# Performance work log

Hardware: AMD Instinct MI355X
Metric: run time of the kernel (lower is better)

Reference implementation:

```python
import jax, jax.numpy as jnp
import numpy as np

B = 256; M = 6; H = 448; INC = 448; EMB = 32; NHEAD = 8; DFF = 2048
OBS = 20; HOR = 30
D = EMB + 4 * NHEAD + INC      # transformer d_model = 512 (requires INC == hidden_dim)
LBUF = OBS + HOR               # 50-token buffer; index 49 is written but never read
HD = D // NHEAD
FUS_IN = D + 7 + INC           # fusion layer input = 71 + 2*hidden_dim


def _ln(x, g, b):
    mu = x.mean(-1, keepdims=True)
    var = ((x - mu) ** 2).mean(-1, keepdims=True)
    return (x - mu) * jax.lax.rsqrt(var + 1e-5) * g + b


def setup_inputs() -> dict:
    key = jax.random.key(0)
    ks = jax.random.split(key, 16)
    s = jnp.float32(0.02)
    n = lambda i, shp: jax.random.normal(ks[i], shp, dtype=jnp.float32)
    return {
        "feat_in": n(0, (B, 1, INC)),
        "loc_in": n(1, (B, M, 2)),
        "obs_trajs": n(2, (OBS, B, 2)),
        "W_emb": n(3, (2, EMB)) * s, "b_emb": jnp.zeros((EMB,)),
        "W_qkv": n(4, (D, 3 * D)) * s, "b_qkv": jnp.zeros((3 * D,)),
        "W_o": n(5, (D, D)) * s, "b_o": jnp.zeros((D,)),
        "W_ff1": n(6, (D, DFF)) * s, "b_ff1": jnp.zeros((DFF,)),
        "W_ff2": n(7, (DFF, D)) * s, "b_ff2": jnp.zeros((D,)),
        "ln1_g": jnp.ones((D,)), "ln1_b": jnp.zeros((D,)),
        "ln2_g": jnp.ones((D,)), "ln2_b": jnp.zeros((D,)),
        "W_fus": n(8, (FUS_IN, H)) * s, "b_fus": jnp.zeros((H,)),
        "W_out": n(9, (H, 2)) * s, "b_out": jnp.zeros((2,)),
    }


def reference(feat_in, loc_in, obs_trajs, W_emb, b_emb, W_qkv, b_qkv, W_o, b_o,
              W_ff1, b_ff1, W_ff2, b_ff2, ln1_g, ln1_b, ln2_g, ln2_b,
              W_fus, b_fus, W_out, b_out):
    feat = feat_in[:, 0]                                     # [B, INC]
    emb_obs = jax.nn.relu(obs_trajs @ W_emb + b_emb)         # [OBS, B, EMB]
    pos0 = jnp.zeros((LBUF, B, 2), feat.dtype).at[:OBS].set(obs_trajs)
    emb0 = jnp.zeros((LBUF, B, EMB), feat.dtype).at[:OBS].set(emb_obs)
    idxs = jnp.arange(OBS, OBS + HOR)
    scale = 1.0 / jnp.sqrt(jnp.float32(HD))
    rep = NHEAD // 2

    def run_sample(goal):                                    # goal: [B, 2]
        def step(carry, frame_idx):
            pos, emb = carry
            last = pos[frame_idx - 1]                        # [B, 2]
            dist = goal - last
            tcol = jnp.zeros((B, 1), feat.dtype) + frame_idx
            # order matches torch.cat: (emb, goal, last, dist, time, feat)
            extras = jnp.concatenate([jnp.tile(goal, (1, rep)), jnp.tile(last, (1, rep)),
                                      jnp.tile(dist, (1, rep)), jnp.tile(tcol, (1, NHEAD))], -1)
            x = jnp.concatenate([emb,
                                 jnp.broadcast_to(extras, (LBUF, B, 4 * NHEAD)),
                                 jnp.broadcast_to(feat, (LBUF, B, INC))], -1)   # [LBUF, B, D]
            qkv = x @ W_qkv + b_qkv
            q, k, v = jnp.split(qkv, 3, axis=-1)
            qh = q[frame_idx - 1].reshape(B, NHEAD, HD)      # only last query needed
            kh = k.reshape(LBUF, B, NHEAD, HD)
            vh = v.reshape(LBUF, B, NHEAD, HD)
            scores = jnp.einsum('bhd,lbhd->bhl', qh, kh) * scale
            valid = jnp.arange(LBUF) < frame_idx             # tokens 0..frame_idx-1 exist
            scores = jnp.where(valid[None, None, :], scores, -1e9)
            attn = jax.nn.softmax(scores, axis=-1)
            ctx = jnp.einsum('bhl,lbhd->bhd', attn, vh).reshape(B, D)
            a = ctx @ W_o + b_o
            x_last = x[frame_idx - 1]
            h1 = _ln(x_last + a, ln1_g, ln1_b)               # post-LN encoder layer (eval, no dropout)
            ff = jax.nn.relu(h1 @ W_ff1 + b_ff1) @ W_ff2 + b_ff2
            h2 = _ln(h1 + ff, ln2_g, ln2_b)
            fus = jnp.concatenate([h2, last, goal, dist, tcol, feat], -1)       # [B, FUS_IN]
            out = (fus @ W_fus + b_fus) @ W_out + b_out                         # [B, 2]
            pos = pos.at[frame_idx].set(out)
            emb = emb.at[frame_idx].set(jax.nn.relu(out @ W_emb + b_emb))
            return (pos, emb), out
        _, ys = jax.lax.scan(step, (pos0, emb0), idxs)
        return ys                                            # [HOR, B, 2]

    ys = jax.vmap(run_sample, in_axes=1)(loc_in)             # [M, HOR, B, 2]
    return ys.transpose(2, 0, 1, 3).reshape(B, M, HOR * 2)
```

## Files before the change

### kernel.cpp

```cpp
#include <hip/hip_runtime.h>
#include <math.h>

#define B_   256
#define N_   1536
#define OBS_ 20
#define HOR_ 30

typedef __bf16 bf16;
typedef bf16  bf16x8 __attribute__((ext_vector_type(8)));
typedef float f32x4  __attribute__((ext_vector_type(4)));

__device__ __forceinline__ void dev_gemm(
    const float* __restrict__ A, int lda,
    const float* __restrict__ Bw, int ldb,
    float* __restrict__ C, bf16* __restrict__ Cb, int ldc,
    int K, const float* __restrict__ colBias,
    int by, int bx, float* smem)
{
    float (*As)[36] = (float(*)[36])smem;
    float (*Bs)[68] = (float(*)[68])(smem + 16 * 36);
    const int tid = threadIdx.x;
    const int n0 = by * 32, j0 = bx * 64;
    const int a_k = tid & 15, a_r = tid >> 4;
    const int b_j = tid & 63, b_k = tid >> 6;
    const int tx = tid & 15, ty = tid >> 4;
    float acc[2][4] = {};
    float pa0 = A[(size_t)(n0 + a_r) * lda + a_k];
    float pa1 = A[(size_t)(n0 + a_r + 16) * lda + a_k];
    float pb[4];
#pragma unroll
    for (int i = 0; i < 4; i++) pb[i] = Bw[(size_t)(b_k + 4 * i) * ldb + j0 + b_j];
    for (int k0 = 0; k0 < K; k0 += 16) {
        As[a_k][a_r] = pa0;
        As[a_k][a_r + 16] = pa1;
#pragma unroll
        for (int i = 0; i < 4; i++) Bs[b_k + 4 * i][b_j] = pb[i];
        __syncthreads();
        if (k0 + 16 < K) {
            pa0 = A[(size_t)(n0 + a_r) * lda + k0 + 16 + a_k];
            pa1 = A[(size_t)(n0 + a_r + 16) * lda + k0 + 16 + a_k];
#pragma unroll
            for (int i = 0; i < 4; i++)
                pb[i] = Bw[(size_t)(k0 + 16 + b_k + 4 * i) * ldb + j0 + b_j];
        }
#pragma unroll
        for (int kk = 0; kk < 16; kk++) {
            float a0 = As[kk][ty * 2];
            float a1 = As[kk][ty * 2 + 1];
            float4 bv = *(const float4*)&Bs[kk][tx * 4];
            float bb[4] = {bv.x, bv.y, bv.z, bv.w};
#pragma unroll
            for (int j = 0; j < 4; j++) { acc[0][j] += a0 * bb[j]; acc[1][j] += a1 * bb[j]; }
        }
        __syncthreads();
    }
#pragma unroll
    for (int i = 0; i < 2; i++) {
        int n = n0 + ty * 2 + i;
#pragma unroll
        for (int j = 0; j < 4; j++) {
            int jj = j0 + tx * 4 + j;
            float v = acc[i][j];
            if (colBias) v += colBias[jj];
            if (C)  C[(size_t)n * ldc + jj] = v;
            if (Cb) Cb[(size_t)n * ldc + jj] = (bf16)v;
        }
    }
}

__device__ __forceinline__ void dev_pack(
    int bi, const float* __restrict__ srcF, const bf16* __restrict__ srcB,
    int srcRows, int KC, int J, int lds, bf16* __restrict__ dst)
{
    int idx = bi * 256 + threadIdx.x;
    int total = (J / 16) * KC * 64;
    if (idx >= total) return;
    int lane = idx & 63;
    int kc = (idx >> 6) % KC;
    int jg = idx / (64 * KC);
    int k0 = kc * 32 + (lane >> 4) * 8;
    int col = jg * 16 + (lane & 15);
    bf16x8 v;
#pragma unroll
    for (int i = 0; i < 8; i++) {
        int r = k0 + i;
        float x = 0.f;
        if (r < srcRows) x = srcF ? srcF[(size_t)r * lds + col] : (float)srcB[(size_t)r * lds + col];
        v[i] = (bf16)x;
    }
    *(bf16x8*)&dst[(size_t)idx * 8] = v;
}

__device__ __forceinline__ void dev_emb_obs(
    int bi, const float* __restrict__ obs, const float* __restrict__ Wemb,
    const float* __restrict__ bemb, float* __restrict__ emb_obs)
{
    int tid = bi * 256 + threadIdx.x;
    if (tid >= OBS_ * B_ * 32) return;
    int r = tid >> 5, e = tid & 31;
    float v = obs[r * 2] * Wemb[e] + obs[r * 2 + 1] * Wemb[32 + e] + bemb[e];
    emb_obs[tid] = fmaxf(v, 0.f);
}

__device__ __forceinline__ void dev_weff(
    int r, const float* __restrict__ Wqkv, const float* __restrict__ bqkv,
    float* __restrict__ Weff, float* smem)
{
    float* qrow = smem;
    const int t = threadIdx.x;
    for (int j = t; j < 512; j += 256)
        qrow[j] = (r < 512) ? Wqkv[(size_t)r * 1536 + j] : bqkv[j];
    __syncthreads();
    const int h = t >> 5, c = t & 31;
    float acc = 0.f;
#pragma unroll 8
    for (int d = 0; d < 64; d++)
        acc += qrow[h * 64 + d] * Wqkv[(size_t)c * 1536 + 512 + h * 64 + d];
    Weff[(size_t)r * 256 + t] = acc;
}

__device__ __forceinline__ void dev_wov(
    int row, const float* __restrict__ Wqkv, const float* __restrict__ Wo,
    bf16* __restrict__ WovCat, float* smem)
{
    float* vrow = smem;
    const int h = row >> 5, c = row & 31;
    const int t = threadIdx.x;
    if (t < 64) vrow[t] = Wqkv[(size_t)c * 1536 + 1024 + h * 64 + t];
    __syncthreads();
    for (int j = t; j < 512; j += 256) {
        float acc = 0.f;
#pragma unroll 8
        for (int d = 0; d < 64; d++)
            acc += vrow[d] * Wo[(size_t)(h * 64 + d) * 512 + j];
        WovCat[(size_t)row * 512 + j] = (bf16)acc;
    }
}

__global__ __launch_bounds__(256) void prologue1_k(
    const float* __restrict__ obs, const float* __restrict__ Wemb,
    const float* __restrict__ bemb, float* __restrict__ emb_obs,
    const float* __restrict__ Wqkv, const float* __restrict__ bqkv,
    float* __restrict__ Weff,
    const float* __restrict__ Wo, bf16* __restrict__ WovCat,
    const float* __restrict__ feat, float* __restrict__ featv,
    const float* __restrict__ Wfus, const float* __restrict__ bfus,
    float* __restrict__ feat_fus,
    const float* __restrict__ Wff1, bf16* __restrict__ BpF1,
    const float* __restrict__ Wff2, bf16* __restrict__ BpF2,
    bf16* __restrict__ BpFus)
{
    __shared__ __attribute__((aligned(16))) float smem[16 * 36 + 16 * 68];
    const int b = blockIdx.x;
    if (b < 640) {
        dev_emb_obs(b, obs, Wemb, bemb, emb_obs);
    } else if (b < 1153) {
        dev_weff(b - 640, Wqkv, bqkv, Weff, smem);
    } else if (b < 1409) {
        dev_wov(b - 1153, Wqkv, Wo, WovCat, smem);
    } else if (b < 1473) {
        int i = b - 1409;
        dev_gemm(feat, 448, Wqkv + 64 * 1536 + 1024, 1536,
                 featv, nullptr, 512, 448, bqkv + 1024, i >> 3, i & 7, smem);
    } else if (b < 1489) {
        int i = b - 1473;
        dev_gemm(Wqkv + 32 * 1536 + 1024, 1536, Wo, 512,
                 nullptr, WovCat + 256 * 512, 512, 512, nullptr, i >> 3, i & 7, smem);
    } else if (b < 1545) {
        int i = b - 1489;
        dev_gemm(feat, 448, Wfus + 519 * 448, 448,
                 feat_fus, nullptr, 448, 448, bfus, i / 7, i % 7, smem);
    } else if (b < 2057) {
        dev_pack(b - 1545, Wff1, nullptr, 512, 16, 2048, 2048, BpF1);
    } else if (b < 2569) {
        dev_pack(b - 2057, Wff2, nullptr, 2048, 64, 512, 512, BpF2);
    } else {
        dev_pack(b - 2569, Wfus, nullptr, 519, 17, 448, 448, BpFus);
    }
}

__global__ __launch_bounds__(256) void prologue2_k(
    const float* __restrict__ feat, const float* __restrict__ Weff,
    float* __restrict__ featqp,
    const float* __restrict__ featv, const float* __restrict__ Wo,
    const float* __restrict__ b_o, float* __restrict__ featvO,
    const bf16* __restrict__ WovCat, bf16* __restrict__ BpA)
{
    __shared__ __attribute__((aligned(16))) float smem[16 * 36 + 16 * 68];
    const int b = blockIdx.x;
    if (b < 32) {
        int i = b;
        dev_gemm(feat, 448, Weff + 64 * 256, 256,
                 featqp, nullptr, 256, 448, Weff + 512 * 256, i >> 2, i & 3, smem);
    } else if (b < 96) {
        int i = b - 32;
        dev_gemm(featv, 512, Wo, 512,
                 featvO, nullptr, 512, 512, b_o, i >> 3, i & 7, smem);
    } else {
        dev_pack(b - 96, nullptr, WovCat, 288, 9, 512, 512, BpA);
    }
}

template<int KC>
__global__ __launch_bounds__(256) void fgemm_k(
    const bf16* __restrict__ A, int lda,
    const bf16* __restrict__ Bp,
    float* __restrict__ C, bf16* __restrict__ Cb, int ldc,
    const float* __restrict__ colBias,
    const float* __restrict__ rowMat, int ldRm,
    int doRelu)
{
    const int n0 = blockIdx.y * 32;
    const int j0g = blockIdx.x * 4;
    const int tid = threadIdx.x;
    const int w = tid >> 6, lane = tid & 63;
    const int quad = lane >> 4, m15 = lane & 15;
    const int r0 = (w & 1) * 16;
    const int cg = (w >> 1) * 2;
    const bf16* Arow = &A[(size_t)(n0 + r0 + m15) * lda + quad * 8];
    const bf16* B0 = &Bp[((size_t)(j0g + cg) * KC * 64 + lane) * 8];
    const bf16* B1 = &Bp[((size_t)(j0g + cg + 1) * KC * 64 + lane) * 8];
    f32x4 acc0 = {}, acc1 = {};
#pragma unroll 8
    for (int kc = 0; kc < KC; kc++) {
        bf16x8 af = *(const bf16x8*)&Arow[kc * 32];
        bf16x8 b0 = *(const bf16x8*)&B0[(size_t)kc * 512];
        bf16x8 b1 = *(const bf16x8*)&B1[(size_t)kc * 512];
        acc0 = __builtin_amdgcn_mfma_f32_16x16x32_bf16(af, b0, acc0, 0, 0, 0);
        acc1 = __builtin_amdgcn_mfma_f32_16x16x32_bf16(af, b1, acc1, 0, 0, 0);
    }
#pragma unroll
    for (int g = 0; g < 2; g++) {
        f32x4 a = g ? acc1 : acc0;
        int j = (j0g + cg + g) * 16 + m15;
        float cb = colBias ? colBias[j] : 0.f;
#pragma unroll
        for (int r = 0; r < 4; r++) {
            int n = n0 + r0 + quad * 4 + r;
            float v = a[r] + cb;
            if (rowMat) v += rowMat[(size_t)(n / 6) * ldRm + j];
            if (doRelu) v = fmaxf(v, 0.f);
            if (C)  C[(size_t)n * ldc + j] = v;
            if (Cb) Cb[(size_t)n * ldc + j] = (bf16)v;
        }
    }
}

__global__ __launch_bounds__(256) void attn_k(
    const float* __restrict__ qp, const float* __restrict__ emb_obs,
    const float* __restrict__ emb_gen, bf16* __restrict__ ecA1b, int t)
{
    __shared__ float qp_s[256];
    __shared__ float emb_s[50 * 33];
    __shared__ float at_s[4][64];
    const int n = blockIdx.x, b = n / 6, tid = threadIdx.x;
    qp_s[tid] = qp[(size_t)n * 256 + tid];
    for (int idx = tid; idx < t * 32; idx += 256) {
        int l = idx >> 5, c = idx & 31;
        emb_s[l * 33 + c] = (l < OBS_) ? emb_obs[((size_t)l * B_ + b) * 32 + c]
                                       : emb_gen[((size_t)(l - OBS_) * N_ + n) * 32 + c];
    }
    __syncthreads();
    const int w = tid >> 6, lane = tid & 63;
#pragma unroll
    for (int hh = 0; hh < 2; hh++) {
        const int h = w * 2 + hh;
        float sc = -1e30f;
        if (lane < t) {
            float s_ = 0.f;
#pragma unroll 8
            for (int c = 0; c < 32; c++) s_ += emb_s[lane * 33 + c] * qp_s[h * 32 + c];
            sc = s_ * 0.125f;
        }
        float mx = sc;
#pragma unroll
        for (int o = 32; o > 0; o >>= 1) mx = fmaxf(mx, __shfl_xor(mx, o, 64));
        float e = (lane < t) ? __expf(sc - mx) : 0.f;
        float sm = e;
#pragma unroll
        for (int o = 32; o > 0; o >>= 1) sm += __shfl_xor(sm, o, 64);
        at_s[w][lane] = e / sm;
        if (lane < 32) {
            float ec = 0.f;
            for (int l = 0; l < t; l++) ec += at_s[w][l] * emb_s[l * 33 + lane];
            ecA1b[(size_t)n * 288 + h * 32 + lane] = (bf16)ec;
        }
    }
}

__global__ __launch_bounds__(256) void ln1_k(
    const float* __restrict__ a, const float* __restrict__ A1f,
    const float* __restrict__ feat, const float* __restrict__ g,
    const float* __restrict__ bt, float* __restrict__ h1f, bf16* __restrict__ h1b)
{
    __shared__ float red[8];
    const int n = blockIdx.x, b = n / 6, tid = threadIdx.x;
    float r[2]; float s = 0.f, sq = 0.f;
#pragma unroll
    for (int i = 0; i < 2; i++) {
        int j = tid + i * 256;
        float x = (j < 64) ? A1f[(size_t)n * 64 + j] : feat[(size_t)b * 448 + (j - 64)];
        float v = a[(size_t)n * 512 + j] + x;
        r[i] = v; s += v; sq += v * v;
    }
#pragma unroll
    for (int o = 32; o > 0; o >>= 1) { s += __shfl_xor(s, o, 64); sq += __shfl_xor(sq, o, 64); }
    int w = tid >> 6, lane = tid & 63;
    if (lane == 0) { red[w] = s; red[4 + w] = sq; }
    __syncthreads();
    s  = red[0] + red[1] + red[2] + red[3];
    sq = red[4] + red[5] + red[6] + red[7];
    float mu = s * (1.f / 512.f);
    float var = sq * (1.f / 512.f) - mu * mu;
    float rs = rsqrtf(var + 1e-5f);
#pragma unroll
    for (int i = 0; i < 2; i++) {
        int j = tid + i * 256;
        float v = (r[i] - mu) * rs * g[j] + bt[j];
        h1f[(size_t)n * 512 + j] = v;
        h1b[(size_t)n * 512 + j] = (bf16)v;
    }
}

__global__ __launch_bounds__(256) void ln2_k(
    const float* __restrict__ h1, const float* __restrict__ ff,
    const float* __restrict__ g, const float* __restrict__ bt,
    const float* __restrict__ small5, bf16* __restrict__ h2p)
{
    __shared__ float red[8];
    const int n = blockIdx.x, tid = threadIdx.x;
    float r[2]; float s = 0.f, sq = 0.f;
#pragma unroll
    for (int i = 0; i < 2; i++) {
        int j = tid + i * 256;
        float v = h1[(size_t)n * 512 + j] + ff[(size_t)n * 512 + j];
        r[i] = v; s += v; sq += v * v;
    }
#pragma unroll
    for (int o = 32; o > 0; o >>= 1) { s += __shfl_xor(s, o, 64); sq += __shfl_xor(sq, o, 64); }
    int w = tid >> 6, lane = tid & 63;
    if (lane == 0) { red[w] = s; red[4 + w] = sq; }
    __syncthreads();
    s  = red[0] + red[1] + red[2] + red[3];
    sq = red[4] + red[5] + red[6] + red[7];
    float mu = s * (1.f / 512.f);
    float var = sq * (1.f / 512.f) - mu * mu;
    float rs = rsqrtf(var + 1e-5f);
#pragma unroll
    for (int i = 0; i < 2; i++) {
        int j = tid + i * 256;
        h2p[(size_t)n * 544 + j] = (bf16)((r[i] - mu) * rs * g[j] + bt[j]);
    }
    if (tid < 7)  h2p[(size_t)n * 544 + 512 + tid] = (bf16)small5[n * 8 + tid];
    if (tid < 25) h2p[(size_t)n * 544 + 519 + tid] = (bf16)0.f;
}

__device__ __forceinline__ void next_state(
    int n, int b, int t, float o0, float o1, float g0, float g1, float tc,
    const float* Wemb, const float* bemb, const float* Weff, const float* featqp,
    float* emb_dst, float* A1f, bf16* ecA1b, float* small5, float* qp, float* A1s)
{
    float d0 = g0 - o0, d1 = g1 - o1;
    if (t < 32) {
        float e = fmaxf(o0 * Wemb[t] + o1 * Wemb[32 + t] + bemb[t], 0.f);
        if (emb_dst) emb_dst[t] = e;
        A1s[t] = e;
    } else if (t < 64) {
        int c = t - 32;
        float v;
        if      (c < 8)  v = (c & 1) ? g1 : g0;
        else if (c < 16) v = (c & 1) ? o1 : o0;
        else if (c < 24) v = (c & 1) ? d1 : d0;
        else             v = tc;
        A1s[t] = v;
    }
    if (t < 7) {
        float v2 = (t==0)?o0:(t==1)?o1:(t==2)?g0:(t==3)?g1:(t==4)?d0:(t==5)?d1:tc;
        small5[n * 8 + t] = v2;
    }
    __syncthreads();
    if (t < 64) {
        A1f[(size_t)n * 64 + t] = A1s[t];
        if (t >= 32) ecA1b[(size_t)n * 288 + 256 + (t - 32)] = (bf16)A1s[t];
    }
    float acc = featqp[(size_t)b * 256 + t];
#pragma unroll 8
    for (int k = 0; k < 64; k++) acc += A1s[k] * Weff[k * 256 + t];
    qp[(size_t)n * 256 + t] = acc;
}

__global__ __launch_bounds__(256) void init_k(
    const float* __restrict__ obs, const float* __restrict__ emb_obs,
    const float* __restrict__ loc, const float* __restrict__ Weff,
    const float* __restrict__ featqp,
    float* __restrict__ A1f, bf16* __restrict__ ecA1b,
    float* __restrict__ small5, float* __restrict__ qp)
{
    __shared__ float A1s[64];
    const int n = blockIdx.x, b = n / 6, m = n % 6, t = threadIdx.x;
    float o0 = obs[(19 * B_ + b) * 2], o1 = obs[(19 * B_ + b) * 2 + 1];
    float g0 = loc[b * 12 + m * 2], g1 = loc[b * 12 + m * 2 + 1];
    if (t < 32) {
        A1s[t] = emb_obs[((size_t)19 * B_ + b) * 32 + t];
    } else if (t < 64) {
        int c = t - 32; float d0 = g0 - o0, d1 = g1 - o1; float tc = 20.f;
        float v;
        if      (c < 8)  v = (c & 1) ? g1 : g0;
        else if (c < 16) v = (c & 1) ? o1 : o0;
        else if (c < 24) v = (c & 1) ? d1 : d0;
        else             v = tc;
        A1s[t] = v;
    }
    if (t < 7) {
        float d0 = g0 - o0, d1 = g1 - o1; float tc = 20.f;
        float v2 = (t==0)?o0:(t==1)?o1:(t==2)?g0:(t==3)?g1:(t==4)?d0:(t==5)?d1:tc;
        small5[n * 8 + t] = v2;
    }
    __syncthreads();
    if (t < 64) {
        A1f[(size_t)n * 64 + t] = A1s[t];
        if (t >= 32) ecA1b[(size_t)n * 288 + 256 + (t - 32)] = (bf16)A1s[t];
    }
    float acc = featqp[(size_t)b * 256 + t];
#pragma unroll 8
    for (int k = 0; k < 64; k++) acc += A1s[k] * Weff[k * 256 + t];
    qp[(size_t)n * 256 + t] = acc;
}

__global__ __launch_bounds__(256) void finish_k(
    const float* __restrict__ fusv, const float* __restrict__ Wout,
    const float* __restrict__ bout, const float* __restrict__ Wemb,
    const float* __restrict__ bemb, const float* __restrict__ loc,
    const float* __restrict__ Weff, const float* __restrict__ featqp,
    float* __restrict__ dout, float* __restrict__ emb_gen,
    float* __restrict__ A1f, bf16* __restrict__ ecA1b,
    float* __restrict__ small5, float* __restrict__ qp, int s)
{
    __shared__ float red[8];
    __shared__ float osh[2];
    __shared__ float A1s[64];
    const int n = blockIdx.x, b = n / 6, m = n % 6, t = threadIdx.x;
    float f0 = fusv[(size_t)n * 448 + t];
    float p0 = f0 * Wout[t * 2];
    float p1 = f0 * Wout[t * 2 + 1];
    if (t < 192) {
        float f1 = fusv[(size_t)n * 448 + 256 + t];
        p0 += f1 * Wout[(256 + t) * 2];
        p1 += f1 * Wout[(256 + t) * 2 + 1];
    }
#pragma unroll
    for (int o = 32; o > 0; o >>= 1) { p0 += __shfl_xor(p0, o, 64); p1 += __shfl_xor(p1, o, 64); }
    int w = t >> 6, lane = t & 63;
    if (lane == 0) { red[w] = p0; red[4 + w] = p1; }
    __syncthreads();
    if (t == 0) {
        float o0 = red[0] + red[1] + red[2] + red[3] + bout[0];
        float o1 = red[4] + red[5] + red[6] + red[7] + bout[1];
        osh[0] = o0; osh[1] = o1;
        dout[(size_t)b * 360 + m * 60 + s * 2]     = o0;
        dout[(size_t)b * 360 + m * 60 + s * 2 + 1] = o1;
    }
    __syncthreads();
    float o0 = osh[0], o1 = osh[1];
    float g0 = loc[b * 12 + m * 2], g1 = loc[b * 12 + m * 2 + 1];
    next_state(n, b, t, o0, o1, g0, g1, (float)(OBS_ + s + 1),
               Wemb, bemb, Weff, featqp,
               &emb_gen[((size_t)s * N_ + n) * 32], A1f, ecA1b, small5, qp, A1s);
}

extern "C" void kernel_launch(void* const* d_in, const int* in_sizes, int n_in,
                              void* d_out_, int out_size, void* d_ws, size_t ws_size,
                              hipStream_t stream) {
    (void)in_sizes; (void)n_in; (void)out_size; (void)ws_size;
    const float* feat  = (const float*)d_in[0];
    const float* loc   = (const float*)d_in[1];
    const float* obs   = (const float*)d_in[2];
    const float* W_emb = (const float*)d_in[3];
    const float* b_emb = (const float*)d_in[4];
    const float* W_qkv = (const float*)d_in[5];
    const float* b_qkv = (const float*)d_in[6];
    const float* W_o   = (const float*)d_in[7];
    const float* b_o   = (const float*)d_in[8];
    const float* W_ff1 = (const float*)d_in[9];
    const float* b_ff1 = (const float*)d_in[10];
    const float* W_ff2 = (const float*)d_in[11];
    const float* b_ff2 = (const float*)d_in[12];
    const float* ln1_g = (const float*)d_in[13];
    const float* ln1_b = (const float*)d_in[14];
    const float* ln2_g = (const float*)d_in[15];
    const float* ln2_b = (const float*)d_in[16];
    const float* W_fus = (const float*)d_in[17];
    const float* b_fus = (const float*)d_in[18];
    const float* W_out = (const float*)d_in[19];
    const float* b_out = (const float*)d_in[20];
    float* dout = (float*)d_out_;

    float* ws = (float*)d_ws;
    float* Weff     = ws; ws += 513 * 256;
    float* featqp   = ws; ws += 256 * 256;
    float* featv    = ws; ws += 256 * 512;
    float* featvO   = ws; ws += 256 * 512;
    float* feat_fus = ws; ws += 256 * 448;
    float* emb_obs  = ws; ws += OBS_ * B_ * 32;
    float* emb_gen  = ws; ws += HOR_ * N_ * 32;
    float* qp       = ws; ws += (size_t)N_ * 256;
    float* A1f      = ws; ws += (size_t)N_ * 64;
    float* small5   = ws; ws += (size_t)N_ * 8;
    float* h1f      = ws; ws += (size_t)N_ * 512;
    float* aF       = ws; ws += (size_t)N_ * 512;
    float* ffB      = ws; ws += (size_t)N_ * 512;
    float* fusv     = ws; ws += (size_t)N_ * 448;
    bf16* WovCat = (bf16*)ws; ws += (320 * 512) / 2;
    bf16* BpA    = (bf16*)ws; ws += (32 * 9 * 512) / 2;
    bf16* BpF1   = (bf16*)ws; ws += (128 * 16 * 512) / 2;
    bf16* BpF2   = (bf16*)ws; ws += (32 * 64 * 512) / 2;
    bf16* BpFus  = (bf16*)ws; ws += (28 * 17 * 512) / 2;
    bf16* ecA1b  = (bf16*)ws; ws += ((size_t)N_ * 288) / 2;
    bf16* h1b    = (bf16*)ws; ws += ((size_t)N_ * 512) / 2;
    bf16* f1b    = (bf16*)ws; ws += ((size_t)N_ * 2048) / 2;
    bf16* h2p    = (bf16*)ws; ws += ((size_t)N_ * 544) / 2;

    prologue1_k<<<dim3(2688), dim3(256), 0, stream>>>(
        obs, W_emb, b_emb, emb_obs, W_qkv, b_qkv, Weff, W_o, WovCat,
        feat, featv, W_fus, b_fus, feat_fus, W_ff1, BpF1, W_ff2, BpF2, BpFus);
    prologue2_k<<<dim3(168), dim3(256), 0, stream>>>(
        feat, Weff, featqp, featv, W_o, b_o, featvO, WovCat, BpA);
    init_k<<<dim3(N_), dim3(256), 0, stream>>>(obs, emb_obs, loc, Weff, featqp,
        A1f, ecA1b, small5, qp);

    for (int s = 0; s < HOR_; s++) {
        attn_k<<<dim3(N_), dim3(256), 0, stream>>>(qp, emb_obs, emb_gen, ecA1b, OBS_ + s);
        fgemm_k<9><<<dim3(8, 48), dim3(256), 0, stream>>>(ecA1b, 288, BpA,
            aF, nullptr, 512, nullptr, featvO, 512, 0);
        ln1_k<<<dim3(N_), dim3(256), 0, stream>>>(aF, A1f, feat, ln1_g, ln1_b, h1f, h1b);
        fgemm_k<16><<<dim3(32, 48), dim3(256), 0, stream>>>(h1b, 512, BpF1,
            nullptr, f1b, 2048, b_ff1, nullptr, 0, 1);
        fgemm_k<64><<<dim3(8, 48), dim3(256), 0, stream>>>(f1b, 2048, BpF2,
            ffB, nullptr, 512, b_ff2, nullptr, 0, 0);
        ln2_k<<<dim3(N_), dim3(256), 0, stream>>>(h1f, ffB, ln2_g, ln2_b, small5, h2p);
        fgemm_k<17><<<dim3(7, 48), dim3(256), 0, stream>>>(h2p, 544, BpFus,
            fusv, nullptr, 448, nullptr, feat_fus, 448, 0);
        finish_k<<<dim3(N_), dim3(256), 0, stream>>>(fusv, W_out, b_out, W_emb, b_emb,
            loc, Weff, featqp, dout, emb_gen, A1f, ecA1b, small5, qp, s);
    }
}
```

Before: 2.686 ms.

## Fuse step-finish into attention and LayerNorm2 into fusion GEMM

Folds the per-step output projection, embedding update and query recompute (formerly finish_k) into the start of the next step's attention kernel, with one trailing finish_k after the loop. Also fuses LayerNorm2 into the fusion-layer MFMA GEMM, so the normalized bf16 rows stay in shared memory instead of going through a global h2p buffer. This removes two kernel launches per step and one global round-trip of activations. In exchange, LN2 is recomputed redundantly across the 7 column blocks, and the attention kernel carries extra serial work.

```diff
diff --git a/kernel.cpp b/kernel.cpp
--- a/kernel.cpp
+++ b/kernel.cpp
@@ -246,27 +246,100 @@
     }
 }
 
-__global__ __launch_bounds__(256) void attn_k(
-    const float* __restrict__ qp, const float* __restrict__ emb_obs,
-    const float* __restrict__ emb_gen, bf16* __restrict__ ecA1b, int t)
+__global__ __launch_bounds__(256) void attn2_k(
+    const float* __restrict__ qp_g,
+    const float* __restrict__ emb_obs,
+    float* __restrict__ emb_gen,
+    const float* __restrict__ fusv,
+    const float* __restrict__ Wout, const float* __restrict__ bout,
+    const float* __restrict__ Wemb, const float* __restrict__ bemb,
+    const float* __restrict__ loc,
+    const float* __restrict__ Weff, const float* __restrict__ featqp,
+    float* __restrict__ dout,
+    float* __restrict__ A1f, bf16* __restrict__ ecA1b,
+    float* __restrict__ small5, int s)
 {
     __shared__ float qp_s[256];
     __shared__ float emb_s[50 * 33];
     __shared__ float at_s[4][64];
-    const int n = blockIdx.x, b = n / 6, tid = threadIdx.x;
-    qp_s[tid] = qp[(size_t)n * 256 + tid];
-    for (int idx = tid; idx < t * 32; idx += 256) {
+    __shared__ float red[8];
+    __shared__ float osh[2];
+    __shared__ float A1s[64];
+    const int n = blockIdx.x, b = n / 6, m = n % 6, tid = threadIdx.x;
+    const int tlen = OBS_ + s;
+
+    if (s == 0) {
+        qp_s[tid] = qp_g[(size_t)n * 256 + tid];
+    } else {
+        float f0 = fusv[(size_t)n * 448 + tid];
+        float p0 = f0 * Wout[tid * 2];
+        float p1 = f0 * Wout[tid * 2 + 1];
+        if (tid < 192) {
+            float f1 = fusv[(size_t)n * 448 + 256 + tid];
+            p0 += f1 * Wout[(256 + tid) * 2];
+            p1 += f1 * Wout[(256 + tid) * 2 + 1];
+        }
+#pragma unroll
+        for (int o = 32; o > 0; o >>= 1) { p0 += __shfl_xor(p0, o, 64); p1 += __shfl_xor(p1, o, 64); }
+        int w = tid >> 6, lane = tid & 63;
+        if (lane == 0) { red[w] = p0; red[4 + w] = p1; }
+        __syncthreads();
+        if (tid == 0) {
+            float o0 = red[0] + red[1] + red[2] + red[3] + bout[0];
+            float o1 = red[4] + red[5] + red[6] + red[7] + bout[1];
+            osh[0] = o0; osh[1] = o1;
+            dout[(size_t)b * 360 + m * 60 + (s - 1) * 2]     = o0;
+            dout[(size_t)b * 360 + m * 60 + (s - 1) * 2 + 1] = o1;
+        }
+        __syncthreads();
+        float o0 = osh[0], o1 = osh[1];
+        float g0 = loc[b * 12 + m * 2], g1 = loc[b * 12 + m * 2 + 1];
+        float d0 = g0 - o0, d1 = g1 - o1;
+        float tc = (float)(OBS_ + s);
+        if (tid < 32) {
+            float e = fmaxf(o0 * Wemb[tid] + o1 * Wemb[32 + tid] + bemb[tid], 0.f);
+            emb_gen[((size_t)(s - 1) * N_ + n) * 32 + tid] = e;
+            A1s[tid] = e;
+        } else if (tid < 64) {
+            int c = tid - 32;
+            float v;
+            if      (c < 8)  v = (c & 1) ? g1 : g0;
+            else if (c < 16) v = (c & 1) ? o1 : o0;
+            else if (c < 24) v = (c & 1) ? d1 : d0;
+            else             v = tc;
+            A1s[tid] = v;
+        }
+        if (tid < 7) {
+            float v2 = (tid==0)?o0:(tid==1)?o1:(tid==2)?g0:(tid==3)?g1:(tid==4)?d0:(tid==5)?d1:tc;
+            small5[n * 8 + tid] = v2;
+        }
+        __syncthreads();
+        if (tid < 64) {
+            A1f[(size_t)n * 64 + tid] = A1s[tid];
+            if (tid >= 32) ecA1b[(size_t)n * 288 + 256 + (tid - 32)] = (bf16)A1s[tid];
+        }
+        float acc = featqp[(size_t)b * 256 + tid];
+#pragma unroll 8
+        for (int k = 0; k < 64; k++) acc += A1s[k] * Weff[k * 256 + tid];
+        qp_s[tid] = acc;
+    }
+
+    for (int idx = tid; idx < tlen * 32; idx += 256) {
         int l = idx >> 5, c = idx & 31;
-        emb_s[l * 33 + c] = (l < OBS_) ? emb_obs[((size_t)l * B_ + b) * 32 + c]
-                                       : emb_gen[((size_t)(l - OBS_) * N_ + n) * 32 + c];
-    }
-    __syncthreads();
+        float v;
+        if (l < OBS_)                 v = emb_obs[((size_t)l * B_ + b) * 32 + c];
+        else if (l == tlen - 1)       v = A1s[c];
+        else                          v = emb_gen[((size_t)(l - OBS_) * N_ + n) * 32 + c];
+        emb_s[l * 33 + c] = v;
+    }
+    __syncthreads();
+
     const int w = tid >> 6, lane = tid & 63;
 #pragma unroll
     for (int hh = 0; hh < 2; hh++) {
         const int h = w * 2 + hh;
         float sc = -1e30f;
-        if (lane < t) {
+        if (lane < tlen) {
             float s_ = 0.f;
 #pragma unroll 8
             for (int c = 0; c < 32; c++) s_ += emb_s[lane * 33 + c] * qp_s[h * 32 + c];
@@ -275,14 +348,14 @@
         float mx = sc;
 #pragma unroll
         for (int o = 32; o > 0; o >>= 1) mx = fmaxf(mx, __shfl_xor(mx, o, 64));
-        float e = (lane < t) ? __expf(sc - mx) : 0.f;
+        float e = (lane < tlen) ? __expf(sc - mx) : 0.f;
         float sm = e;
 #pragma unroll
         for (int o = 32; o > 0; o >>= 1) sm += __shfl_xor(sm, o, 64);
         at_s[w][lane] = e / sm;
         if (lane < 32) {
             float ec = 0.f;
-            for (int l = 0; l < t; l++) ec += at_s[w][l] * emb_s[l * 33 + lane];
+            for (int l = 0; l < tlen; l++) ec += at_s[w][l] * emb_s[l * 33 + lane];
             ecA1b[(size_t)n * 288 + h * 32 + lane] = (bf16)ec;
         }
     }
@@ -322,37 +395,76 @@
     }
 }
 
-__global__ __launch_bounds__(256) void ln2_k(
-    const float* __restrict__ h1, const float* __restrict__ ff,
-    const float* __restrict__ g, const float* __restrict__ bt,
-    const float* __restrict__ small5, bf16* __restrict__ h2p)
-{
-    __shared__ float red[8];
-    const int n = blockIdx.x, tid = threadIdx.x;
-    float r[2]; float s = 0.f, sq = 0.f;
-#pragma unroll
-    for (int i = 0; i < 2; i++) {
-        int j = tid + i * 256;
-        float v = h1[(size_t)n * 512 + j] + ff[(size_t)n * 512 + j];
-        r[i] = v; s += v; sq += v * v;
-    }
-#pragma unroll
-    for (int o = 32; o > 0; o >>= 1) { s += __shfl_xor(s, o, 64); sq += __shfl_xor(sq, o, 64); }
-    int w = tid >> 6, lane = tid & 63;
-    if (lane == 0) { red[w] = s; red[4 + w] = sq; }
-    __syncthreads();
-    s  = red[0] + red[1] + red[2] + red[3];
-    sq = red[4] + red[5] + red[6] + red[7];
-    float mu = s * (1.f / 512.f);
-    float var = sq * (1.f / 512.f) - mu * mu;
-    float rs = rsqrtf(var + 1e-5f);
-#pragma unroll
-    for (int i = 0; i < 2; i++) {
-        int j = tid + i * 256;
-        h2p[(size_t)n * 544 + j] = (bf16)((r[i] - mu) * rs * g[j] + bt[j]);
-    }
-    if (tid < 7)  h2p[(size_t)n * 544 + 512 + tid] = (bf16)small5[n * 8 + tid];
-    if (tid < 25) h2p[(size_t)n * 544 + 519 + tid] = (bf16)0.f;
+__global__ __launch_bounds__(512) void fusln_k(
+    const float* __restrict__ h1f, const float* __restrict__ ffB,
+    const float* __restrict__ g2, const float* __restrict__ bt2,
+    const float* __restrict__ small5,
+    const bf16* __restrict__ Bp,
+    const float* __restrict__ feat_fus,
+    float* __restrict__ fusv)
+{
+    __shared__ __attribute__((aligned(16))) bf16 h2s[32][552];
+    const int n0 = blockIdx.y * 32;
+    const int j0g = blockIdx.x * 4;
+    const int tid = threadIdx.x;
+
+    {
+        const int row = tid >> 4, li = tid & 15;
+        const int n = n0 + row;
+        float v32[32];
+        float s_ = 0.f, sq = 0.f;
+        const float* h1p = &h1f[(size_t)n * 512 + li * 32];
+        const float* ffp = &ffB[(size_t)n * 512 + li * 32];
+#pragma unroll
+        for (int i4 = 0; i4 < 8; i4++) {
+            float4 a4 = *(const float4*)&h1p[i4 * 4];
+            float4 b4 = *(const float4*)&ffp[i4 * 4];
+            float x0 = a4.x + b4.x, x1 = a4.y + b4.y, x2 = a4.z + b4.z, x3 = a4.w + b4.w;
+            v32[i4 * 4 + 0] = x0; v32[i4 * 4 + 1] = x1; v32[i4 * 4 + 2] = x2; v32[i4 * 4 + 3] = x3;
+            s_ += x0 + x1 + x2 + x3;
+            sq += x0 * x0 + x1 * x1 + x2 * x2 + x3 * x3;
+        }
+#pragma unroll
+        for (int o = 1; o < 16; o <<= 1) { s_ += __shfl_xor(s_, o, 64); sq += __shfl_xor(sq, o, 64); }
+        float mu = s_ * (1.f / 512.f);
+        float var = sq * (1.f / 512.f) - mu * mu;
+        float rs = rsqrtf(var + 1e-5f);
+#pragma unroll
+        for (int i = 0; i < 32; i++) {
+            int c = li * 32 + i;
+            h2s[row][c] = (bf16)((v32[i] - mu) * rs * g2[c] + bt2[c]);
+        }
+        if (tid < 32) {
+#pragma unroll
+            for (int sl = 0; sl < 32; sl++) {
+                float vt = (sl < 7) ? small5[(size_t)(n0 + tid) * 8 + sl] : 0.f;
+                h2s[tid][512 + sl] = (bf16)vt;
+            }
+        }
+    }
+    __syncthreads();
+
+    {
+        const int w = tid >> 6, lane = tid & 63;
+        const int quad = lane >> 4, m15 = lane & 15;
+        const int r0 = (w & 1) * 16;
+        const int cg = w >> 1;
+        const bf16* Bb = &Bp[((size_t)(j0g + cg) * 17 * 64 + lane) * 8];
+        f32x4 acc = {};
+#pragma unroll
+        for (int kc = 0; kc < 17; kc++) {
+            bf16x8 af = *(const bf16x8*)&h2s[r0 + m15][kc * 32 + quad * 8];
+            bf16x8 bg = *(const bf16x8*)&Bb[(size_t)kc * 512];
+            acc = __builtin_amdgcn_mfma_f32_16x16x32_bf16(af, bg, acc, 0, 0, 0);
+        }
+        int j = (j0g + cg) * 16 + m15;
+#pragma unroll
+        for (int r = 0; r < 4; r++) {
+            int n = n0 + r0 + quad * 4 + r;
+            float v = acc[r] + feat_fus[(size_t)(n / 6) * 448 + j];
+            fusv[(size_t)n * 448 + j] = v;
+        }
+    }
 }
 
 __device__ __forceinline__ void next_state(
@@ -518,7 +630,6 @@
     bf16* ecA1b  = (bf16*)ws; ws += ((size_t)N_ * 288) / 2;
     bf16* h1b    = (bf16*)ws; ws += ((size_t)N_ * 512) / 2;
     bf16* f1b    = (bf16*)ws; ws += ((size_t)N_ * 2048) / 2;
-    bf16* h2p    = (bf16*)ws; ws += ((size_t)N_ * 544) / 2;
 
     prologue1_k<<<dim3(2688), dim3(256), 0, stream>>>(
         obs, W_emb, b_emb, emb_obs, W_qkv, b_qkv, Weff, W_o, WovCat,
@@ -529,7 +640,9 @@
         A1f, ecA1b, small5, qp);
 
     for (int s = 0; s < HOR_; s++) {
-        attn_k<<<dim3(N_), dim3(256), 0, stream>>>(qp, emb_obs, emb_gen, ecA1b, OBS_ + s);
+        attn2_k<<<dim3(N_), dim3(256), 0, stream>>>(qp, emb_obs, emb_gen, fusv,
+            W_out, b_out, W_emb, b_emb, loc, Weff, featqp,
+            dout, A1f, ecA1b, small5, s);
         fgemm_k<9><<<dim3(8, 48), dim3(256), 0, stream>>>(ecA1b, 288, BpA,
             aF, nullptr, 512, nullptr, featvO, 512, 0);
         ln1_k<<<dim3(N_), dim3(256), 0, stream>>>(aF, A1f, feat, ln1_g, ln1_b, h1f, h1b);
@@ -537,10 +650,9 @@
             nullptr, f1b, 2048, b_ff1, nullptr, 0, 1);
         fgemm_k<64><<<dim3(8, 48), dim3(256), 0, stream>>>(f1b, 2048, BpF2,
             ffB, nullptr, 512, b_ff2, nullptr, 0, 0);
-        ln2_k<<<dim3(N_), dim3(256), 0, stream>>>(h1f, ffB, ln2_g, ln2_b, small5, h2p);
-        fgemm_k<17><<<dim3(7, 48), dim3(256), 0, stream>>>(h2p, 544, BpFus,
-            fusv, nullptr, 448, nullptr, feat_fus, 448, 0);
-        finish_k<<<dim3(N_), dim3(256), 0, stream>>>(fusv, W_out, b_out, W_emb, b_emb,
-            loc, Weff, featqp, dout, emb_gen, A1f, ecA1b, small5, qp, s);
-    }
-}
+        fusln_k<<<dim3(7, 48), dim3(512), 0, stream>>>(h1f, ffB, ln2_g, ln2_b,
+            small5, BpFus, feat_fus, fusv);
+    }
+    finish_k<<<dim3(N_), dim3(256), 0, stream>>>(fusv, W_out, b_out, W_emb, b_emb,
+        loc, Weff, featqp, dout, emb_gen, A1f, ecA1b, small5, qp, 29);
+}
```

Measured after the change: 2.924 ms. +8.8%, slower.
